# Kernel optimization log

Measured on AMD Instinct MI355X. Metric: run time of the kernel, lower is better.

Reference implementation:

```python
import jax, jax.numpy as jnp
import numpy as np

N = 50000      # total nodes across batched subgraphs
E = 800000     # total edges
R = 4          # num_relations
G = 16         # number of graphs (questions) in batch
NODE_DIM = 128
QDIM = 768
RQ = 64        # reduced_qn_dim
RN = 64        # reduced_node_dim
H = 128        # hidden_dim
OUT = 64       # output_dim


def setup_inputs() -> dict:
    key = jax.random.key(0)
    ks = jax.random.split(key, 16)
    def lin(k, i, o):
        return jax.random.normal(k, (i, o), jnp.float32) / np.float32(np.sqrt(i))
    def rel(k, i, o):
        return jax.random.normal(k, (R, i, o), jnp.float32) / np.float32(np.sqrt(i))
    return {
        "x": jax.random.normal(ks[0], (N, NODE_DIM), jnp.float32),
        "edge_index": jax.random.randint(ks[1], (2, E), 0, N, dtype=jnp.int32),
        "edge_attr": jax.random.randint(ks[2], (E,), 0, R, dtype=jnp.int32),
        "batch": jnp.sort(jax.random.randint(ks[3], (N,), 0, G, dtype=jnp.int32)),
        "question_embedding": jax.random.normal(ks[4], (G, QDIM), jnp.float32),
        "qn_W": lin(ks[5], QDIM, RQ), "qn_b": jnp.zeros((RQ,), jnp.float32),
        "W0": rel(ks[6], NODE_DIM, RN), "root0": lin(ks[7], NODE_DIM, RN), "b0": jnp.zeros((RN,), jnp.float32),
        "W1": rel(ks[8], RN + RQ, H), "root1": lin(ks[9], RN + RQ, H), "b1": jnp.zeros((H,), jnp.float32),
        "W2": rel(ks[10], H, H), "root2": lin(ks[11], H, H), "b2": jnp.zeros((H,), jnp.float32),
        "W3": rel(ks[12], H, OUT), "root3": lin(ks[13], H, OUT), "b3": jnp.zeros((OUT,), jnp.float32),
    }


def rgcn_conv(x, src, dst, etype, W, root, b):
    """PyG RGCNConv: out_i = x_i @ root + b + sum_r mean_{j in N_r(i)} x_j @ W_r."""
    out = x @ root + b
    for r in range(R):
        h = x @ W[r]                                  # [N, out] transform-then-gather
        mask = (etype == r)
        msgs = jnp.where(mask[:, None], h[src], 0.0)  # [E, out]
        s = jax.ops.segment_sum(msgs, dst, num_segments=N)
        cnt = jax.ops.segment_sum(mask.astype(x.dtype), dst, num_segments=N)
        out = out + s / jnp.maximum(cnt, 1.0)[:, None]
    return out


def reference(x, edge_index, edge_attr, batch, question_embedding,
              qn_W, qn_b, W0, root0, b0, W1, root1, b1, W2, root2, b2, W3, root3, b3):
    src, dst = edge_index[0], edge_index[1]
    q = jax.nn.relu(question_embedding @ qn_W + qn_b)          # [G, RQ]
    h = jax.nn.relu(rgcn_conv(x, src, dst, edge_attr, W0, root0, b0))
    combined = jnp.concatenate([h, q[batch]], axis=1)          # [N, RN+RQ]
    h = jax.nn.relu(rgcn_conv(combined, src, dst, edge_attr, W1, root1, b1))
    h = jax.nn.relu(rgcn_conv(h, src, dst, edge_attr, W2, root2, b2))
    return rgcn_conv(h, src, dst, edge_attr, W3, root3, b3)
```

## Files before the change

### kernel.cpp

```cpp
#include <hip/hip_runtime.h>
#include <hip/hip_bf16.h>

#define NN 50000
#define EE 800000
#define GG 16
#define QD 768
#define NBUCK 196
#define EPB 4000

typedef __bf16 bf16x8 __attribute__((ext_vector_type(8)));
typedef float f32x4 __attribute__((ext_vector_type(4)));

static __device__ __forceinline__ float bflo(unsigned u) {
    union { unsigned v; float f; } c; c.v = u << 16; return c.f;
}
static __device__ __forceinline__ float bfhi(unsigned u) {
    union { unsigned v; float f; } c; c.v = u & 0xffff0000u; return c.f;
}


#define PB_CVT 6250
#define PB_W0  (PB_CVT + 160)
#define PB_W1  (PB_W0 + 320)
#define PB_W2  (PB_W1 + 320)
#define PB_W3  (PB_W2 + 160)
#define PB_Q   (PB_W3 + 16)

__global__ __launch_bounds__(256) void prep_all(
        const float* __restrict__ x, __hip_bfloat16* __restrict__ xb,
        const float* __restrict__ qe, const float* __restrict__ qn_W,
        const float* __restrict__ qn_b, float* __restrict__ q,
        const float* __restrict__ W0, const float* __restrict__ root0, __hip_bfloat16* __restrict__ W5T0,
        const float* __restrict__ W1, const float* __restrict__ root1, __hip_bfloat16* __restrict__ W5T1,
        const float* __restrict__ W2, const float* __restrict__ root2, __hip_bfloat16* __restrict__ W5T2,
        const float* __restrict__ W3, const float* __restrict__ root3, __hip_bfloat16* __restrict__ W5T3) {
    __shared__ float red[256];
    int blk = blockIdx.x, tid = threadIdx.x;
    if (blk < PB_CVT) {
        int i = blk * 256 + tid;
        float4 v = ((const float4*)x)[i];
        union { ushort4 u; __hip_bfloat16 h[4]; } o;
        o.h[0] = __float2bfloat16(v.x); o.h[1] = __float2bfloat16(v.y);
        o.h[2] = __float2bfloat16(v.z); o.h[3] = __float2bfloat16(v.w);
        ((ushort4*)xb)[i] = o.u;
    } else if (blk < PB_W3) {
        const float* W; const float* root; __hip_bfloat16* WT; int O, base;
        if (blk < PB_W0)      { W = W0; root = root0; WT = W5T0; O = 64;  base = PB_CVT; }
        else if (blk < PB_W1) { W = W1; root = root1; WT = W5T1; O = 128; base = PB_W0; }
        else if (blk < PB_W2) { W = W2; root = root2; WT = W5T2; O = 128; base = PB_W1; }
        else                  { W = W3; root = root3; WT = W5T3; O = 64;  base = PB_W2; }
        int idx = (blk - base) * 256 + tid;
        int o = idx / 640, k = idx - o * 640;
        float v;
        if (k < 128) v = root[(size_t)k * O + o];
        else { int r = (k - 128) >> 7, kk = (k - 128) & 127; v = W[((size_t)r * 128 + kk) * O + o]; }
        WT[idx] = __float2bfloat16(v);
    } else {
        int g = blk - PB_W3;
        int o = tid & 63, kc = tid >> 6;
        const float* qr = qe + (size_t)g * QD;
        float s = 0.f;
        int k0 = kc * 192;
        for (int k = k0; k < k0 + 192; ++k)
            s = fmaf(qr[k], qn_W[(size_t)k * 64 + o], s);
        red[tid] = s;
        __syncthreads();
        if (tid < 64) {
            float t = red[tid] + red[tid + 64] + red[tid + 128] + red[tid + 192] + qn_b[o];
            q[g * 64 + o] = fmaxf(t, 0.f);
        }
    }
}


__global__ void bucket_hist(const int* __restrict__ dst, int* __restrict__ bcnt) {
    __shared__ int h[NBUCK];
    int tid = threadIdx.x;
    for (int i = tid; i < NBUCK; i += 256) h[i] = 0;
    __syncthreads();
    for (int e = blockIdx.x * 256 + tid; e < EE; e += gridDim.x * 256)
        atomicAdd(&h[dst[e] >> 8], 1);
    __syncthreads();
    for (int i = tid; i < NBUCK; i += 256) if (h[i]) atomicAdd(&bcnt[i], h[i]);
}

__global__ void bucket_scan(const int* __restrict__ bcnt, int* __restrict__ bbase,
                            int* __restrict__ bcur) {
    __shared__ int wt[4];
    int tid = threadIdx.x, lane = tid & 63, w = tid >> 6;
    int v = (tid < NBUCK) ? bcnt[tid] : 0;
    int sc = v;
#pragma unroll
    for (int off = 1; off < 64; off <<= 1) {
        int t = __shfl_up(sc, off, 64);
        if (lane >= off) sc += t;
    }
    if (lane == 63) wt[w] = sc;
    __syncthreads();
    int wbase = 0;
    for (int ww = 0; ww < w; ++ww) wbase += wt[ww];
    int excl = wbase + sc - v;
    if (tid <= NBUCK) bbase[tid] = excl;
    if (tid < NBUCK) bcur[tid] = excl;
}

__global__ __launch_bounds__(256) void bin_edges(const int* __restrict__ src,
                                                 const int* __restrict__ dst,
                                                 const int* __restrict__ et,
                                                 int* __restrict__ bcur,
                                                 unsigned* __restrict__ binned) {
    __shared__ int lcnt[NBUCK];
    __shared__ int lbase[NBUCK];
    int tid = threadIdx.x;
    int e0 = blockIdx.x * EPB, e1 = min(e0 + EPB, EE);
    for (int base = e0; base < e1; base += 2048) {
        for (int i = tid; i < NBUCK; i += 256) lcnt[i] = 0;
        __syncthreads();
        unsigned ent[8]; int bk[8], rk[8];
#pragma unroll
        for (int k = 0; k < 8; ++k) {
            int e = base + k * 256 + tid;
            if (e < e1) {
                int d = dst[e];
                bk[k] = d >> 8;
                ent[k] = ((unsigned)src[e] << 10) | ((unsigned)et[e] << 8) | (unsigned)(d & 255);
                rk[k] = atomicAdd(&lcnt[bk[k]], 1);
            } else bk[k] = -1;
        }
        __syncthreads();
        for (int i = tid; i < NBUCK; i += 256)
            lbase[i] = lcnt[i] ? atomicAdd(&bcur[i], lcnt[i]) : 0;
        __syncthreads();
#pragma unroll
        for (int k = 0; k < 8; ++k)
            if (bk[k] >= 0) binned[lbase[bk[k]] + rk[k]] = ent[k];
        __syncthreads();
    }
}

__global__ __launch_bounds__(256) void csr_fine(const int* __restrict__ bbase,
                                                const unsigned* __restrict__ binned,
                                                int* __restrict__ csr,
                                                int* __restrict__ offsets,
                                                int4* __restrict__ cnt4) {
    __shared__ int cnt[1024];
    __shared__ int wt[4];
    int b = blockIdx.x, tid = threadIdx.x, lane = tid & 63, w = tid >> 6;
    int seg0 = bbase[b], seg1 = bbase[b + 1];
    for (int i = tid; i < 1024; i += 256) cnt[i] = 0;
    __syncthreads();
    for (int e = seg0 + tid; e < seg1; e += 256) {
        unsigned u = binned[e];
        atomicAdd(&cnt[(u & 255) * 4 + ((u >> 8) & 3)], 1);
    }
    __syncthreads();
    int c0 = cnt[tid * 4], c1 = cnt[tid * 4 + 1], c2 = cnt[tid * 4 + 2], c3 = cnt[tid * 4 + 3];
    int s = c0 + c1 + c2 + c3;
    int sc = s;
#pragma unroll
    for (int off = 1; off < 64; off <<= 1) {
        int t = __shfl_up(sc, off, 64);
        if (lane >= off) sc += t;
    }
    if (lane == 63) wt[w] = sc;
    __syncthreads();
    int wbase = 0;
    for (int ww = 0; ww < w; ++ww) wbase += wt[ww];
    int excl = wbase + sc - s;
    cnt[tid * 4]     = excl;
    cnt[tid * 4 + 1] = excl + c0;
    cnt[tid * 4 + 2] = excl + c0 + c1;
    cnt[tid * 4 + 3] = excl + c0 + c1 + c2;
    int node = b * 256 + tid;
    if (node < NN) {
        offsets[node] = seg0 + excl;
        cnt4[node] = make_int4(c0, c1, c2, c3);
    }
    if (b == NBUCK - 1 && tid == 0) offsets[NN] = EE;
    __syncthreads();
    for (int e = seg0 + tid; e < seg1; e += 256) {
        unsigned u = binned[e];
        int r = atomicAdd(&cnt[(u & 255) * 4 + ((u >> 8) & 3)], 1);
        csr[seg0 + r] = (int)(((u >> 10) << 2) | ((u >> 8) & 3));
    }
}


__global__ __launch_bounds__(256) void agg_x(const __hip_bfloat16* __restrict__ X,
                                             const int* __restrict__ offsets,
                                             const int4* __restrict__ cnt4,
                                             const int* __restrict__ csr,
                                             const float* __restrict__ zpage,
                                             __hip_bfloat16* __restrict__ X5agg) {
    int lane = threadIdx.x & 63;
    int node = __builtin_amdgcn_readfirstlane(blockIdx.x * 4 + (threadIdx.x >> 6));
    const char* xb = (const char*)X;
    const char* zp = (const char*)zpage;
    int e0 = offsets[node];
    int4 c4 = cnt4[node];
    int st[4];
    st[0] = 0; st[1] = c4.x; st[2] = st[1] + c4.y; st[3] = st[2] + c4.z;
    int cs[4] = {c4.x, c4.y, c4.z, c4.w};
    int maxc = max(max(cs[0], cs[1]), max(cs[2], cs[3]));
    float aL[4] = {0.f, 0.f, 0.f, 0.f}, aH[4] = {0.f, 0.f, 0.f, 0.f};
    for (int i = 0; i < maxc; i += 2) {
        const char* bp[8];
#pragma unroll
        for (int jj = 0; jj < 2; ++jj) {
            int i2 = i + jj;
#pragma unroll
            for (int r = 0; r < 4; ++r) {
                int p = csr[min(e0 + st[r] + i2, EE - 1)];
                bp[jj * 4 + r] = (i2 < cs[r]) ? xb + (size_t)(p >> 2) * 256 : zp;
            }
        }
        unsigned u[8];
#pragma unroll
        for (int k = 0; k < 8; ++k)
            u[k] = *(const unsigned*)(bp[k] + lane * 4);
#pragma unroll
        for (int k = 0; k < 8; ++k) {
            int r = k & 3;
            aL[r] += bflo(u[k]);
            aH[r] += bfhi(u[k]);
        }
    }
    char* x5 = (char*)X5agg;
#pragma unroll
    for (int r = 0; r < 4; ++r) {
        float iv = 1.f / fmaxf((float)cs[r], 1.f);
        __hip_bfloat16 g0 = __float2bfloat16(aL[r] * iv);
        __hip_bfloat16 g1 = __float2bfloat16(aH[r] * iv);
        ushort2 pkd;
        pkd.x = *(unsigned short*)&g0; pkd.y = *(unsigned short*)&g1;
        *(ushort2*)(x5 + (size_t)node * 1024 + r * 256 + lane * 4) = pkd;
    }
}


template <int O, int MODE>
__global__ __launch_bounds__(256) void dense5(const __hip_bfloat16* __restrict__ Xself,
                                              const __hip_bfloat16* __restrict__ X5agg,
                                              const __hip_bfloat16* __restrict__ W5T,
                                              const float* __restrict__ bias,
                                              const float* __restrict__ q,
                                              const int* __restrict__ batch,
                                              __hip_bfloat16* __restrict__ xnext,
                                              float* __restrict__ out) {
    __shared__ char lds[16384];
    constexpr int NCT = O / 16;
    int tid = threadIdx.x;
    int wave = tid >> 6, lane = tid & 63;
    int quad = lane >> 4, l15 = lane & 15;
    int mbase = blockIdx.x * 128 + wave * 32;
    const __bf16* Ws = (const __bf16*)W5T;

    f32x4 acc[2][NCT];
#pragma unroll
    for (int mt = 0; mt < 2; ++mt)
#pragma unroll
        for (int t = 0; t < NCT; ++t) acc[mt][t] = f32x4{0, 0, 0, 0};

    int arow0 = min(mbase + l15, NN - 1);
    int arow1 = min(mbase + 16 + l15, NN - 1);
    const __bf16* aps0 = (const __bf16*)Xself + (size_t)arow0 * 128;
    const __bf16* aps1 = (const __bf16*)Xself + (size_t)arow1 * 128;
    const __bf16* apg0 = (const __bf16*)X5agg + (size_t)arow0 * 512;
    const __bf16* apg1 = (const __bf16*)X5agg + (size_t)arow1 * 512;

    for (int kc = 0; kc < 10; ++kc) {
        int k0 = kc * 64;
        const __bf16* a0base = (kc < 2) ? aps0 + kc * 64 : apg0 + (kc - 2) * 64;
        const __bf16* a1base = (kc < 2) ? aps1 + kc * 64 : apg1 + (kc - 2) * 64;
        __syncthreads();
        constexpr int NF = NCT * 2 * 64;
#pragma unroll
        for (int i = 0; i < NF / 256; ++i) {
            int f = tid + i * 256;
            int fl = f & 63;
            int o = (f >> 7) * 16 + (fl & 15);
            int kk = k0 + ((f >> 6) & 1) * 32 + ((fl >> 4) & 3) * 8;
            *(uint4*)(lds + f * 16) = *(const uint4*)(Ws + (size_t)o * 640 + kk);
        }
        __syncthreads();
#pragma unroll
        for (int ks = 0; ks < 2; ++ks) {
            bf16x8 a0 = *(const bf16x8*)(a0base + ks * 32 + quad * 8);
            bf16x8 a1 = *(const bf16x8*)(a1base + ks * 32 + quad * 8);
#pragma unroll
            for (int t = 0; t < NCT; ++t) {
                bf16x8 b = *(const bf16x8*)(lds + ((t * 2 + ks) * 64 + lane) * 16);
                acc[0][t] = __builtin_amdgcn_mfma_f32_16x16x32_bf16(a0, b, acc[0][t], 0, 0, 0);
                acc[1][t] = __builtin_amdgcn_mfma_f32_16x16x32_bf16(a1, b, acc[1][t], 0, 0, 0);
            }
        }
    }
    __syncthreads();

    if (MODE == 2) {
#pragma unroll
        for (int mt = 0; mt < 2; ++mt)
#pragma unroll
            for (int t = 0; t < NCT; ++t) {
                int col = t * 16 + l15;
                float bv = bias[col];
#pragma unroll
                for (int reg = 0; reg < 4; ++reg) {
                    int row = mbase + mt * 16 + quad * 4 + reg;
                    if (row < NN) out[(size_t)row * 64 + col] = acc[mt][t][reg] + bv;
                }
            }
        return;
    }

    __hip_bfloat16* tp = (__hip_bfloat16*)(lds + wave * 4096);
#pragma unroll
    for (int mt = 0; mt < 2; ++mt) {
        int m0 = mbase + mt * 16;
#pragma unroll
        for (int t = 0; t < NCT; ++t) {
            int col = t * 16 + l15;
            float bv = bias[col];
#pragma unroll
            for (int reg = 0; reg < 4; ++reg)
                tp[(quad * 4 + reg) * 128 + col] =
                    __float2bfloat16(fmaxf(acc[mt][t][reg] + bv, 0.f));
        }
        if (MODE == 0) {
            int row = lane >> 2;
            int cs = (lane & 3) * 16;
            int rnode = min(m0 + row, NN - 1);
            int g = batch[rnode];
#pragma unroll
            for (int i = 0; i < 4; ++i) {
                float4 v = *(const float4*)(q + g * 64 + cs + i * 4);
                __hip_bfloat16 q0 = __float2bfloat16(v.x), q1 = __float2bfloat16(v.y);
                __hip_bfloat16 q2 = __float2bfloat16(v.z), q3 = __float2bfloat16(v.w);
                ushort4 pk;
                pk.x = *(unsigned short*)&q0; pk.y = *(unsigned short*)&q1;
                pk.z = *(unsigned short*)&q2; pk.w = *(unsigned short*)&q3;
                *(ushort4*)(tp + row * 128 + 64 + cs + i * 4) = pk;
            }
        }
#pragma unroll
        for (int p = 0; p < 4; ++p) {
            int c = p * 64 + lane;
            int row = m0 + (c >> 4);
            if (row < NN)
                *(uint4*)((char*)xnext + (size_t)row * 256 + (c & 15) * 16) =
                    *(const uint4*)((const char*)tp + c * 16);
        }
    }
}


static inline size_t rup(size_t x) { return (x + 255) & ~(size_t)255; }

extern "C" void kernel_launch(void* const* d_in, const int* in_sizes, int n_in,
                              void* d_out, int out_size, void* d_ws, size_t ws_size,
                              hipStream_t stream) {
    const float* x      = (const float*)d_in[0];
    const int*   esrc   = (const int*)d_in[1];
    const int*   edst   = esrc + EE;
    const int*   eattr  = (const int*)d_in[2];
    const int*   batch  = (const int*)d_in[3];
    const float* qe     = (const float*)d_in[4];
    const float* qn_W   = (const float*)d_in[5];
    const float* qn_b   = (const float*)d_in[6];
    const float* W0 = (const float*)d_in[7],  *root0 = (const float*)d_in[8],  *b0 = (const float*)d_in[9];
    const float* W1 = (const float*)d_in[10], *root1 = (const float*)d_in[11], *b1 = (const float*)d_in[12];
    const float* W2 = (const float*)d_in[13], *root2 = (const float*)d_in[14], *b2 = (const float*)d_in[15];
    const float* W3 = (const float*)d_in[16], *root3 = (const float*)d_in[17], *b3 = (const float*)d_in[18];
    float* out = (float*)d_out;

    char* w = (char*)d_ws;
    float* q       = (float*)w;  w += rup(GG * 64 * 4);
    float* zpage   = (float*)w;  w += rup(256);
    int*   offsets = (int*)w;    w += rup(((size_t)NN + 1) * 4);
    int4*  cnt4    = (int4*)w;   w += rup((size_t)NN * 16);
    int*   bcnt    = (int*)w;    w += rup((size_t)NBUCK * 4);
    int*   bbase   = (int*)w;    w += rup(((size_t)NBUCK + 1) * 4);
    int*   bcur    = (int*)w;    w += rup((size_t)NBUCK * 4);
    unsigned* binned = (unsigned*)w; w += rup((size_t)EE * 4);
    int*   csr     = (int*)w;    w += rup((size_t)EE * 4);
    __hip_bfloat16* W5T0 = (__hip_bfloat16*)w; w += rup((size_t)64 * 640 * 2);
    __hip_bfloat16* W5T1 = (__hip_bfloat16*)w; w += rup((size_t)128 * 640 * 2);
    __hip_bfloat16* W5T2 = (__hip_bfloat16*)w; w += rup((size_t)128 * 640 * 2);
    __hip_bfloat16* W5T3 = (__hip_bfloat16*)w; w += rup((size_t)64 * 640 * 2);
    __hip_bfloat16* xb0 = (__hip_bfloat16*)w;  w += rup((size_t)NN * 128 * 2);
    __hip_bfloat16* xb1 = (__hip_bfloat16*)w;  w += rup((size_t)NN * 128 * 2);
    __hip_bfloat16* X5  = (__hip_bfloat16*)w;  w += rup((size_t)NN * 512 * 2);

    hipMemsetAsync(bcnt, 0, (size_t)NBUCK * 4, stream);
    hipMemsetAsync(zpage, 0, 256, stream);

    prep_all<<<PB_Q, 256, 0, stream>>>(x, xb0, qe, qn_W, qn_b, q,
                                       W0, root0, W5T0, W1, root1, W5T1,
                                       W2, root2, W5T2, W3, root3, W5T3);

    bucket_hist<<<256, 256, 0, stream>>>(edst, bcnt);
    bucket_scan<<<1, 256, 0, stream>>>(bcnt, bbase, bcur);
    bin_edges<<<(EE + EPB - 1) / EPB, 256, 0, stream>>>(esrc, edst, eattr, bcur, binned);
    csr_fine<<<NBUCK, 256, 0, stream>>>(bbase, binned, csr, offsets, cnt4);

    int aggblk = NN / 4;
    int dblk = (NN + 127) / 128;

    agg_x<<<aggblk, 256, 0, stream>>>(xb0, offsets, cnt4, csr, zpage, X5);
    dense5<64, 0><<<dblk, 256, 0, stream>>>(xb0, X5, W5T0, b0, q, batch, xb1, nullptr);

    agg_x<<<aggblk, 256, 0, stream>>>(xb1, offsets, cnt4, csr, zpage, X5);
    dense5<128, 1><<<dblk, 256, 0, stream>>>(xb1, X5, W5T1, b1, nullptr, nullptr, xb0, nullptr);

    agg_x<<<aggblk, 256, 0, stream>>>(xb0, offsets, cnt4, csr, zpage, X5);
    dense5<128, 1><<<dblk, 256, 0, stream>>>(xb0, X5, W5T2, b2, nullptr, nullptr, xb1, nullptr);

    agg_x<<<aggblk, 256, 0, stream>>>(xb1, offsets, cnt4, csr, zpage, X5);
    dense5<64, 2><<<dblk, 256, 0, stream>>>(xb1, X5, W5T3, b3, nullptr, nullptr, nullptr, out);
}
```

Before: 396.4 us.

## Persistent aggregation waves with prefetched CSR metadata and merged histogram launch

The aggregation kernel becomes a grid-stride persistent kernel where each wave prefetches the next node's offsets, counts and first 64 CSR entries per relation while processing the current node. Neighbour indices are loaded once per 64 edges as a vector and broadcast with readlane, replacing per-edge scalar CSR loads, and the gather is unrolled to 16 rows per step. The bucket histogram is folded into the prep kernel to drop one launch. The costs are higher register pressure from the prefetched metadata and the larger unroll, and possible tail imbalance from the fixed grid size.

After: 417.9 us. 5.4% more time.

```diff
diff --git a/kernel.cpp b/kernel.cpp
--- a/kernel.cpp
+++ b/kernel.cpp
@@ -8,6 +8,9 @@
 #define NBUCK 196
 #define EPB 4000
 
+#define AGG_GRID 2048
+#define AGG_STRIDE (AGG_GRID * 4)
+
 typedef __bf16 bf16x8 __attribute__((ext_vector_type(8)));
 typedef float f32x4 __attribute__((ext_vector_type(4)));
 
@@ -25,15 +28,17 @@
 #define PB_W2  (PB_W1 + 320)
 #define PB_W3  (PB_W2 + 160)
 #define PB_Q   (PB_W3 + 16)
-
-__global__ __launch_bounds__(256) void prep_all(
+#define PB_HIST (PB_Q + 256)
+
+__global__ __launch_bounds__(256) void prep_hist(
         const float* __restrict__ x, __hip_bfloat16* __restrict__ xb,
         const float* __restrict__ qe, const float* __restrict__ qn_W,
         const float* __restrict__ qn_b, float* __restrict__ q,
         const float* __restrict__ W0, const float* __restrict__ root0, __hip_bfloat16* __restrict__ W5T0,
         const float* __restrict__ W1, const float* __restrict__ root1, __hip_bfloat16* __restrict__ W5T1,
         const float* __restrict__ W2, const float* __restrict__ root2, __hip_bfloat16* __restrict__ W5T2,
-        const float* __restrict__ W3, const float* __restrict__ root3, __hip_bfloat16* __restrict__ W5T3) {
+        const float* __restrict__ W3, const float* __restrict__ root3, __hip_bfloat16* __restrict__ W5T3,
+        const int* __restrict__ edst, int* __restrict__ bcnt) {
     __shared__ float red[256];
     int blk = blockIdx.x, tid = threadIdx.x;
     if (blk < PB_CVT) {
@@ -55,7 +60,7 @@
         if (k < 128) v = root[(size_t)k * O + o];
         else { int r = (k - 128) >> 7, kk = (k - 128) & 127; v = W[((size_t)r * 128 + kk) * O + o]; }
         WT[idx] = __float2bfloat16(v);
-    } else {
+    } else if (blk < PB_Q) {
         int g = blk - PB_W3;
         int o = tid & 63, kc = tid >> 6;
         const float* qr = qe + (size_t)g * QD;
@@ -69,20 +74,18 @@
             float t = red[tid] + red[tid + 64] + red[tid + 128] + red[tid + 192] + qn_b[o];
             q[g * 64 + o] = fmaxf(t, 0.f);
         }
-    }
-}
-
-
-__global__ void bucket_hist(const int* __restrict__ dst, int* __restrict__ bcnt) {
-    __shared__ int h[NBUCK];
-    int tid = threadIdx.x;
-    for (int i = tid; i < NBUCK; i += 256) h[i] = 0;
-    __syncthreads();
-    for (int e = blockIdx.x * 256 + tid; e < EE; e += gridDim.x * 256)
-        atomicAdd(&h[dst[e] >> 8], 1);
-    __syncthreads();
-    for (int i = tid; i < NBUCK; i += 256) if (h[i]) atomicAdd(&bcnt[i], h[i]);
-}
+    } else {
+        __shared__ int h[NBUCK];
+        int hb = blk - PB_Q;
+        for (int i = tid; i < NBUCK; i += 256) h[i] = 0;
+        __syncthreads();
+        for (int e = hb * 256 + tid; e < EE; e += 256 * 256)
+            atomicAdd(&h[edst[e] >> 8], 1);
+        __syncthreads();
+        for (int i = tid; i < NBUCK; i += 256) if (h[i]) atomicAdd(&bcnt[i], h[i]);
+    }
+}
+
 
 __global__ void bucket_scan(const int* __restrict__ bcnt, int* __restrict__ bbase,
                             int* __restrict__ bcur) {
@@ -186,6 +189,11 @@
 }
 
 
+struct AggMeta {
+    int e0, cs0, cs1, cs2, cs3, maxc;
+    int pk0, pk1, pk2, pk3;
+};
+
 __global__ __launch_bounds__(256) void agg_x(const __hip_bfloat16* __restrict__ X,
                                              const int* __restrict__ offsets,
                                              const int4* __restrict__ cnt4,
@@ -193,47 +201,86 @@
                                              const float* __restrict__ zpage,
                                              __hip_bfloat16* __restrict__ X5agg) {
     int lane = threadIdx.x & 63;
-    int node = __builtin_amdgcn_readfirstlane(blockIdx.x * 4 + (threadIdx.x >> 6));
+    int gw = blockIdx.x * 4 + (threadIdx.x >> 6);
     const char* xb = (const char*)X;
     const char* zp = (const char*)zpage;
-    int e0 = offsets[node];
-    int4 c4 = cnt4[node];
-    int st[4];
-    st[0] = 0; st[1] = c4.x; st[2] = st[1] + c4.y; st[3] = st[2] + c4.z;
-    int cs[4] = {c4.x, c4.y, c4.z, c4.w};
-    int maxc = max(max(cs[0], cs[1]), max(cs[2], cs[3]));
-    float aL[4] = {0.f, 0.f, 0.f, 0.f}, aH[4] = {0.f, 0.f, 0.f, 0.f};
-    for (int i = 0; i < maxc; i += 2) {
-        const char* bp[8];
-#pragma unroll
-        for (int jj = 0; jj < 2; ++jj) {
-            int i2 = i + jj;
-#pragma unroll
-            for (int r = 0; r < 4; ++r) {
-                int p = csr[min(e0 + st[r] + i2, EE - 1)];
-                bp[jj * 4 + r] = (i2 < cs[r]) ? xb + (size_t)(p >> 2) * 256 : zp;
+
+    auto load_meta = [&](int n, AggMeta& m) {
+        int node = __builtin_amdgcn_readfirstlane(n);
+        m.e0 = __builtin_amdgcn_readfirstlane(offsets[node]);
+        int4 c4 = cnt4[node];
+        m.cs0 = __builtin_amdgcn_readfirstlane(c4.x);
+        m.cs1 = __builtin_amdgcn_readfirstlane(c4.y);
+        m.cs2 = __builtin_amdgcn_readfirstlane(c4.z);
+        m.cs3 = __builtin_amdgcn_readfirstlane(c4.w);
+        m.maxc = max(max(m.cs0, m.cs1), max(m.cs2, m.cs3));
+        int st1 = m.cs0, st2 = st1 + m.cs1, st3 = st2 + m.cs2;
+        m.pk0 = csr[min(m.e0 + lane, EE - 1)];
+        m.pk1 = csr[min(m.e0 + st1 + lane, EE - 1)];
+        m.pk2 = csr[min(m.e0 + st2 + lane, EE - 1)];
+        m.pk3 = csr[min(m.e0 + st3 + lane, EE - 1)];
+    };
+
+    auto process = [&](int n, const AggMeta& m) {
+        int node = __builtin_amdgcn_readfirstlane(n);
+        int cs[4] = {m.cs0, m.cs1, m.cs2, m.cs3};
+        int st[4];
+        st[0] = 0; st[1] = cs[0]; st[2] = st[1] + cs[1]; st[3] = st[2] + cs[2];
+        float aL[4] = {0.f, 0.f, 0.f, 0.f}, aH[4] = {0.f, 0.f, 0.f, 0.f};
+        int pk[4] = {m.pk0, m.pk1, m.pk2, m.pk3};
+        for (int base = 0; base < m.maxc; base += 64) {
+            if (base) {
+#pragma unroll
+                for (int r = 0; r < 4; ++r)
+                    pk[r] = csr[min(m.e0 + st[r] + base + lane, EE - 1)];
             }
-        }
-        unsigned u[8];
-#pragma unroll
-        for (int k = 0; k < 8; ++k)
-            u[k] = *(const unsigned*)(bp[k] + lane * 4);
-#pragma unroll
-        for (int k = 0; k < 8; ++k) {
-            int r = k & 3;
-            aL[r] += bflo(u[k]);
-            aH[r] += bfhi(u[k]);
-        }
-    }
-    char* x5 = (char*)X5agg;
-#pragma unroll
-    for (int r = 0; r < 4; ++r) {
-        float iv = 1.f / fmaxf((float)cs[r], 1.f);
-        __hip_bfloat16 g0 = __float2bfloat16(aL[r] * iv);
-        __hip_bfloat16 g1 = __float2bfloat16(aH[r] * iv);
-        ushort2 pkd;
-        pkd.x = *(unsigned short*)&g0; pkd.y = *(unsigned short*)&g1;
-        *(ushort2*)(x5 + (size_t)node * 1024 + r * 256 + lane * 4) = pkd;
+            int mm = min(64, m.maxc - base);
+            for (int j = 0; j < mm; j += 4) {
+                const char* bp[16];
+#pragma unroll
+                for (int jj = 0; jj < 4; ++jj) {
+                    int i = base + j + jj;
+#pragma unroll
+                    for (int r = 0; r < 4; ++r) {
+                        int pv = __builtin_amdgcn_readlane(pk[r], j + jj);
+                        bp[jj * 4 + r] = (i < cs[r]) ? xb + (size_t)(pv >> 2) * 256 : zp;
+                    }
+                }
+                unsigned u[16];
+#pragma unroll
+                for (int k = 0; k < 16; ++k)
+                    u[k] = *(const unsigned*)(bp[k] + lane * 4);
+#pragma unroll
+                for (int k = 0; k < 16; ++k) {
+                    int r = k & 3;
+                    aL[r] += bflo(u[k]);
+                    aH[r] += bfhi(u[k]);
+                }
+            }
+        }
+        char* x5 = (char*)X5agg;
+#pragma unroll
+        for (int r = 0; r < 4; ++r) {
+            float iv = 1.f / fmaxf((float)cs[r], 1.f);
+            __hip_bfloat16 g0 = __float2bfloat16(aL[r] * iv);
+            __hip_bfloat16 g1 = __float2bfloat16(aH[r] * iv);
+            ushort2 pkd;
+            pkd.x = *(unsigned short*)&g0; pkd.y = *(unsigned short*)&g1;
+            *(ushort2*)(x5 + (size_t)node * 1024 + r * 256 + lane * 4) = pkd;
+        }
+    };
+
+    AggMeta m;
+    int n = gw;
+    load_meta(n, m);
+    while (true) {
+        int n2 = n + AGG_STRIDE;
+        bool has2 = (n2 < NN);
+        AggMeta m2;
+        if (has2) load_meta(n2, m2);
+        process(n, m);
+        if (!has2) break;
+        n = n2; m = m2;
     }
 }
 
@@ -394,27 +441,26 @@
     hipMemsetAsync(bcnt, 0, (size_t)NBUCK * 4, stream);
     hipMemsetAsync(zpage, 0, 256, stream);
 
-    prep_all<<<PB_Q, 256, 0, stream>>>(x, xb0, qe, qn_W, qn_b, q,
-                                       W0, root0, W5T0, W1, root1, W5T1,
-                                       W2, root2, W5T2, W3, root3, W5T3);
-
-    bucket_hist<<<256, 256, 0, stream>>>(edst, bcnt);
+    prep_hist<<<PB_HIST, 256, 0, stream>>>(x, xb0, qe, qn_W, qn_b, q,
+                                           W0, root0, W5T0, W1, root1, W5T1,
+                                           W2, root2, W5T2, W3, root3, W5T3,
+                                           edst, bcnt);
+
     bucket_scan<<<1, 256, 0, stream>>>(bcnt, bbase, bcur);
     bin_edges<<<(EE + EPB - 1) / EPB, 256, 0, stream>>>(esrc, edst, eattr, bcur, binned);
     csr_fine<<<NBUCK, 256, 0, stream>>>(bbase, binned, csr, offsets, cnt4);
 
-    int aggblk = NN / 4;
     int dblk = (NN + 127) / 128;
 
-    agg_x<<<aggblk, 256, 0, stream>>>(xb0, offsets, cnt4, csr, zpage, X5);
+    agg_x<<<AGG_GRID, 256, 0, stream>>>(xb0, offsets, cnt4, csr, zpage, X5);
     dense5<64, 0><<<dblk, 256, 0, stream>>>(xb0, X5, W5T0, b0, q, batch, xb1, nullptr);
 
-    agg_x<<<aggblk, 256, 0, stream>>>(xb1, offsets, cnt4, csr, zpage, X5);
+    agg_x<<<AGG_GRID, 256, 0, stream>>>(xb1, offsets, cnt4, csr, zpage, X5);
     dense5<128, 1><<<dblk, 256, 0, stream>>>(xb1, X5, W5T1, b1, nullptr, nullptr, xb0, nullptr);
 
-    agg_x<<<aggblk, 256, 0, stream>>>(xb0, offsets, cnt4, csr, zpage, X5);
+    agg_x<<<AGG_GRID, 256, 0, stream>>>(xb0, offsets, cnt4, csr, zpage, X5);
     dense5<128, 1><<<dblk, 256, 0, stream>>>(xb0, X5, W5T2, b2, nullptr, nullptr, xb1, nullptr);
 
-    agg_x<<<aggblk, 256, 0, stream>>>(xb1, offsets, cnt4, csr, zpage, X5);
+    agg_x<<<AGG_GRID, 256, 0, stream>>>(xb1, offsets, cnt4, csr, zpage, X5);
     dense5<64, 2><<<dblk, 256, 0, stream>>>(xb1, X5, W5T3, b3, nullptr, nullptr, nullptr, out);
 }
```

## Batch CSR index loads per wave and fuse histogram into prep kernel

Applied to the files above, without the earlier changes.

The aggregation kernel now loads up to 64 CSR entries per relation with one coalesced vector load and broadcasts them through readlane, instead of issuing scalar-ish index loads every two neighbors. It unrolls four neighbors per relation per step, giving 16 outstanding gathers. It also uses a grid-stride persistent grid and points out-of-range slots at a zero row appended after the node table, replacing the separate zero page. The bucket histogram and the zeroing are folded into the prep kernel to cut launches and a memset. The cost is extra registers and a fixed grid size that may limit occupancy.

Result: faster. 381.5 us (-3.7%).

```diff
diff --git a/kernel.cpp b/kernel.cpp
--- a/kernel.cpp
+++ b/kernel.cpp
@@ -8,6 +8,9 @@
 #define NBUCK 196
 #define EPB 4000
 
+#define AGG_GRID 2048
+#define AGG_STRIDE (AGG_GRID * 4)
+
 typedef __bf16 bf16x8 __attribute__((ext_vector_type(8)));
 typedef float f32x4 __attribute__((ext_vector_type(4)));
 
@@ -25,15 +28,19 @@
 #define PB_W2  (PB_W1 + 320)
 #define PB_W3  (PB_W2 + 160)
 #define PB_Q   (PB_W3 + 16)
-
-__global__ __launch_bounds__(256) void prep_all(
-        const float* __restrict__ x, __hip_bfloat16* __restrict__ xb,
+#define PB_Z   (PB_Q + 1)
+#define PB_HIST (PB_Z + 256)
+
+__global__ __launch_bounds__(256) void prep_hist(
+        const float* __restrict__ x, __hip_bfloat16* __restrict__ xb0e,
+        __hip_bfloat16* __restrict__ xb1e,
         const float* __restrict__ qe, const float* __restrict__ qn_W,
         const float* __restrict__ qn_b, float* __restrict__ q,
         const float* __restrict__ W0, const float* __restrict__ root0, __hip_bfloat16* __restrict__ W5T0,
         const float* __restrict__ W1, const float* __restrict__ root1, __hip_bfloat16* __restrict__ W5T1,
         const float* __restrict__ W2, const float* __restrict__ root2, __hip_bfloat16* __restrict__ W5T2,
-        const float* __restrict__ W3, const float* __restrict__ root3, __hip_bfloat16* __restrict__ W5T3) {
+        const float* __restrict__ W3, const float* __restrict__ root3, __hip_bfloat16* __restrict__ W5T3,
+        const int* __restrict__ edst, int* __restrict__ bcnt) {
     __shared__ float red[256];
     int blk = blockIdx.x, tid = threadIdx.x;
     if (blk < PB_CVT) {
@@ -42,7 +49,7 @@
         union { ushort4 u; __hip_bfloat16 h[4]; } o;
         o.h[0] = __float2bfloat16(v.x); o.h[1] = __float2bfloat16(v.y);
         o.h[2] = __float2bfloat16(v.z); o.h[3] = __float2bfloat16(v.w);
-        ((ushort4*)xb)[i] = o.u;
+        ((ushort4*)xb0e)[i] = o.u;
     } else if (blk < PB_W3) {
         const float* W; const float* root; __hip_bfloat16* WT; int O, base;
         if (blk < PB_W0)      { W = W0; root = root0; WT = W5T0; O = 64;  base = PB_CVT; }
@@ -55,7 +62,7 @@
         if (k < 128) v = root[(size_t)k * O + o];
         else { int r = (k - 128) >> 7, kk = (k - 128) & 127; v = W[((size_t)r * 128 + kk) * O + o]; }
         WT[idx] = __float2bfloat16(v);
-    } else {
+    } else if (blk < PB_Q) {
         int g = blk - PB_W3;
         int o = tid & 63, kc = tid >> 6;
         const float* qr = qe + (size_t)g * QD;
@@ -69,20 +76,23 @@
             float t = red[tid] + red[tid + 64] + red[tid + 128] + red[tid + 192] + qn_b[o];
             q[g * 64 + o] = fmaxf(t, 0.f);
         }
-    }
-}
-
-
-__global__ void bucket_hist(const int* __restrict__ dst, int* __restrict__ bcnt) {
-    __shared__ int h[NBUCK];
-    int tid = threadIdx.x;
-    for (int i = tid; i < NBUCK; i += 256) h[i] = 0;
-    __syncthreads();
-    for (int e = blockIdx.x * 256 + tid; e < EE; e += gridDim.x * 256)
-        atomicAdd(&h[dst[e] >> 8], 1);
-    __syncthreads();
-    for (int i = tid; i < NBUCK; i += 256) if (h[i]) atomicAdd(&bcnt[i], h[i]);
-}
+    } else if (blk < PB_Z) {
+        if (tid < 64) {
+            ((unsigned*)((char*)xb0e + (size_t)NN * 256))[tid] = 0u;
+            ((unsigned*)((char*)xb1e + (size_t)NN * 256))[tid] = 0u;
+        }
+    } else {
+        __shared__ int h[NBUCK];
+        int hb = blk - PB_Z;
+        for (int i = tid; i < NBUCK; i += 256) h[i] = 0;
+        __syncthreads();
+        for (int e = hb * 256 + tid; e < EE; e += 256 * 256)
+            atomicAdd(&h[edst[e] >> 8], 1);
+        __syncthreads();
+        for (int i = tid; i < NBUCK; i += 256) if (h[i]) atomicAdd(&bcnt[i], h[i]);
+    }
+}
+
 
 __global__ void bucket_scan(const int* __restrict__ bcnt, int* __restrict__ bbase,
                             int* __restrict__ bcur) {
@@ -190,50 +200,62 @@
                                              const int* __restrict__ offsets,
                                              const int4* __restrict__ cnt4,
                                              const int* __restrict__ csr,
-                                             const float* __restrict__ zpage,
                                              __hip_bfloat16* __restrict__ X5agg) {
     int lane = threadIdx.x & 63;
-    int node = __builtin_amdgcn_readfirstlane(blockIdx.x * 4 + (threadIdx.x >> 6));
+    int gw = blockIdx.x * 4 + (threadIdx.x >> 6);
     const char* xb = (const char*)X;
-    const char* zp = (const char*)zpage;
-    int e0 = offsets[node];
-    int4 c4 = cnt4[node];
-    int st[4];
-    st[0] = 0; st[1] = c4.x; st[2] = st[1] + c4.y; st[3] = st[2] + c4.z;
-    int cs[4] = {c4.x, c4.y, c4.z, c4.w};
-    int maxc = max(max(cs[0], cs[1]), max(cs[2], cs[3]));
-    float aL[4] = {0.f, 0.f, 0.f, 0.f}, aH[4] = {0.f, 0.f, 0.f, 0.f};
-    for (int i = 0; i < maxc; i += 2) {
-        const char* bp[8];
-#pragma unroll
-        for (int jj = 0; jj < 2; ++jj) {
-            int i2 = i + jj;
-#pragma unroll
-            for (int r = 0; r < 4; ++r) {
-                int p = csr[min(e0 + st[r] + i2, EE - 1)];
-                bp[jj * 4 + r] = (i2 < cs[r]) ? xb + (size_t)(p >> 2) * 256 : zp;
+    int laneoff = lane * 4;
+    for (int n0 = gw; n0 < NN; n0 += AGG_STRIDE) {
+        int node = __builtin_amdgcn_readfirstlane(n0);
+        int e0 = __builtin_amdgcn_readfirstlane(offsets[node]);
+        int4 c4 = cnt4[node];
+        int cs0 = __builtin_amdgcn_readfirstlane(c4.x);
+        int cs1 = __builtin_amdgcn_readfirstlane(c4.y);
+        int cs2 = __builtin_amdgcn_readfirstlane(c4.z);
+        int cs3 = __builtin_amdgcn_readfirstlane(c4.w);
+        int st1 = cs0, st2 = st1 + cs1, st3 = st2 + cs2;
+        int maxc = max(max(cs0, cs1), max(cs2, cs3));
+        float aL[4] = {0.f, 0.f, 0.f, 0.f}, aH[4] = {0.f, 0.f, 0.f, 0.f};
+        for (int base = 0; base < maxc; base += 64) {
+            int pk0 = csr[min(e0 + base + lane, EE - 1)];
+            int pk1 = csr[min(e0 + st1 + base + lane, EE - 1)];
+            int pk2 = csr[min(e0 + st2 + base + lane, EE - 1)];
+            int pk3 = csr[min(e0 + st3 + base + lane, EE - 1)];
+            int mm = min(64, maxc - base);
+            for (int j = 0; j < mm; j += 4) {
+                unsigned u[16];
+#pragma unroll
+                for (int jj = 0; jj < 4; ++jj) {
+                    int i = base + j + jj;
+                    int sl = j + jj;
+                    int r0 = (i < cs0) ? (__builtin_amdgcn_readlane(pk0, sl) >> 2) : NN;
+                    int r1 = (i < cs1) ? (__builtin_amdgcn_readlane(pk1, sl) >> 2) : NN;
+                    int r2 = (i < cs2) ? (__builtin_amdgcn_readlane(pk2, sl) >> 2) : NN;
+                    int r3 = (i < cs3) ? (__builtin_amdgcn_readlane(pk3, sl) >> 2) : NN;
+                    u[jj * 4 + 0] = *(const unsigned*)(xb + ((size_t)(unsigned)r0 << 8) + laneoff);
+                    u[jj * 4 + 1] = *(const unsigned*)(xb + ((size_t)(unsigned)r1 << 8) + laneoff);
+                    u[jj * 4 + 2] = *(const unsigned*)(xb + ((size_t)(unsigned)r2 << 8) + laneoff);
+                    u[jj * 4 + 3] = *(const unsigned*)(xb + ((size_t)(unsigned)r3 << 8) + laneoff);
+                }
+#pragma unroll
+                for (int k = 0; k < 16; ++k) {
+                    int r = k & 3;
+                    aL[r] += bflo(u[k]);
+                    aH[r] += bfhi(u[k]);
+                }
             }
         }
-        unsigned u[8];
-#pragma unroll
-        for (int k = 0; k < 8; ++k)
-            u[k] = *(const unsigned*)(bp[k] + lane * 4);
-#pragma unroll
-        for (int k = 0; k < 8; ++k) {
-            int r = k & 3;
-            aL[r] += bflo(u[k]);
-            aH[r] += bfhi(u[k]);
-        }
-    }
-    char* x5 = (char*)X5agg;
-#pragma unroll
-    for (int r = 0; r < 4; ++r) {
-        float iv = 1.f / fmaxf((float)cs[r], 1.f);
-        __hip_bfloat16 g0 = __float2bfloat16(aL[r] * iv);
-        __hip_bfloat16 g1 = __float2bfloat16(aH[r] * iv);
-        ushort2 pkd;
-        pkd.x = *(unsigned short*)&g0; pkd.y = *(unsigned short*)&g1;
-        *(ushort2*)(x5 + (size_t)node * 1024 + r * 256 + lane * 4) = pkd;
+        char* x5 = (char*)X5agg;
+        int csa[4] = {cs0, cs1, cs2, cs3};
+#pragma unroll
+        for (int r = 0; r < 4; ++r) {
+            float iv = 1.f / fmaxf((float)csa[r], 1.f);
+            __hip_bfloat16 g0 = __float2bfloat16(aL[r] * iv);
+            __hip_bfloat16 g1 = __float2bfloat16(aH[r] * iv);
+            ushort2 pkd;
+            pkd.x = *(unsigned short*)&g0; pkd.y = *(unsigned short*)&g1;
+            *(ushort2*)(x5 + (size_t)node * 1024 + r * 256 + lane * 4) = pkd;
+        }
     }
 }
 
@@ -375,7 +397,6 @@
 
     char* w = (char*)d_ws;
     float* q       = (float*)w;  w += rup(GG * 64 * 4);
-    float* zpage   = (float*)w;  w += rup(256);
     int*   offsets = (int*)w;    w += rup(((size_t)NN + 1) * 4);
     int4*  cnt4    = (int4*)w;   w += rup((size_t)NN * 16);
     int*   bcnt    = (int*)w;    w += rup((size_t)NBUCK * 4);
@@ -387,34 +408,32 @@
     __hip_bfloat16* W5T1 = (__hip_bfloat16*)w; w += rup((size_t)128 * 640 * 2);
     __hip_bfloat16* W5T2 = (__hip_bfloat16*)w; w += rup((size_t)128 * 640 * 2);
     __hip_bfloat16* W5T3 = (__hip_bfloat16*)w; w += rup((size_t)64 * 640 * 2);
-    __hip_bfloat16* xb0 = (__hip_bfloat16*)w;  w += rup((size_t)NN * 128 * 2);
-    __hip_bfloat16* xb1 = (__hip_bfloat16*)w;  w += rup((size_t)NN * 128 * 2);
+    __hip_bfloat16* xb0 = (__hip_bfloat16*)w;  w += rup(((size_t)NN + 1) * 128 * 2);
+    __hip_bfloat16* xb1 = (__hip_bfloat16*)w;  w += rup(((size_t)NN + 1) * 128 * 2);
     __hip_bfloat16* X5  = (__hip_bfloat16*)w;  w += rup((size_t)NN * 512 * 2);
 
     hipMemsetAsync(bcnt, 0, (size_t)NBUCK * 4, stream);
-    hipMemsetAsync(zpage, 0, 256, stream);
-
-    prep_all<<<PB_Q, 256, 0, stream>>>(x, xb0, qe, qn_W, qn_b, q,
-                                       W0, root0, W5T0, W1, root1, W5T1,
-                                       W2, root2, W5T2, W3, root3, W5T3);
-
-    bucket_hist<<<256, 256, 0, stream>>>(edst, bcnt);
+
+    prep_hist<<<PB_HIST, 256, 0, stream>>>(x, xb0, xb1, qe, qn_W, qn_b, q,
+                                           W0, root0, W5T0, W1, root1, W5T1,
+                                           W2, root2, W5T2, W3, root3, W5T3,
+                                           edst, bcnt);
+
     bucket_scan<<<1, 256, 0, stream>>>(bcnt, bbase, bcur);
     bin_edges<<<(EE + EPB - 1) / EPB, 256, 0, stream>>>(esrc, edst, eattr, bcur, binned);
     csr_fine<<<NBUCK, 256, 0, stream>>>(bbase, binned, csr, offsets, cnt4);
 
-    int aggblk = NN / 4;
     int dblk = (NN + 127) / 128;
 
-    agg_x<<<aggblk, 256, 0, stream>>>(xb0, offsets, cnt4, csr, zpage, X5);
+    agg_x<<<AGG_GRID, 256, 0, stream>>>(xb0, offsets, cnt4, csr, X5);
     dense5<64, 0><<<dblk, 256, 0, stream>>>(xb0, X5, W5T0, b0, q, batch, xb1, nullptr);
 
-    agg_x<<<aggblk, 256, 0, stream>>>(xb1, offsets, cnt4, csr, zpage, X5);
+    agg_x<<<AGG_GRID, 256, 0, stream>>>(xb1, offsets, cnt4, csr, X5);
     dense5<128, 1><<<dblk, 256, 0, stream>>>(xb1, X5, W5T1, b1, nullptr, nullptr, xb0, nullptr);
 
-    agg_x<<<aggblk, 256, 0, stream>>>(xb0, offsets, cnt4, csr, zpage, X5);
+    agg_x<<<AGG_GRID, 256, 0, stream>>>(xb0, offsets, cnt4, csr, X5);
     dense5<128, 1><<<dblk, 256, 0, stream>>>(xb0, X5, W5T2, b2, nullptr, nullptr, xb1, nullptr);
 
-    agg_x<<<aggblk, 256, 0, stream>>>(xb1, offsets, cnt4, csr, zpage, X5);
+    agg_x<<<AGG_GRID, 256, 0, stream>>>(xb1, offsets, cnt4, csr, X5);
     dense5<64, 2><<<dblk, 256, 0, stream>>>(xb1, X5, W5T3, b3, nullptr, nullptr, nullptr, out);
 }
```
